# Performance work log

Measured on AMD Instinct MI355X. Metric: run time of the kernel, lower is better.

Reference implementation:

```python
import jax, jax.numpy as jnp
import numpy as np

B, D = 512, 512

def setup_inputs() -> dict:
    key = jax.random.key(0)
    k1, k2, k3, k4 = jax.random.split(key, 4)
    return {
        "img_proj": jax.random.normal(k1, (B, D), dtype=jnp.float32),
        "audio_proj": jax.random.normal(k2, (B, D), dtype=jnp.float32),
        "W": jax.random.normal(k3, (D, D), dtype=jnp.float32) * 0.02,
        "b": jax.random.normal(k4, (D,), dtype=jnp.float32) * 0.02,
    }

def reference(img_proj, audio_proj, W, b):
    # concat of raw projections (saved before img_proj is transformed)
    concat_proj = jnp.concatenate([img_proj, audio_proj], axis=-1)  # [B, 2D]
    # linear + tanh on image projection
    img_t = jnp.tanh(img_proj @ W.T + b)                            # [B, D]
    # rank-1 bilinear co-attention map: L[b,i,j] = img_t[b,i] * audio[b,j]
    L = img_t[:, :, None] * audio_proj[:, None, :]                  # [B, D, D]
    # softmax over dim=1 (rows), attend audio: C_img[b,e] = sum_d audio[b,d] * S1[b,e,d]
    S1 = jax.nn.softmax(L, axis=1)
    C_img = jnp.einsum('bd,bed->be', audio_proj, S1)                # [B, D]
    # softmax over dim=2 (cols), attend tanh-image: C_audio[b,e] = sum_d img_t[b,d] * S2[b,d,e]
    S2 = jax.nn.softmax(L, axis=2)
    C_audio = jnp.einsum('bd,bde->be', img_t, S2)                   # [B, D]
    fused = jnp.concatenate([C_img, C_audio], axis=-1)              # [B, 2D]
    return jnp.concatenate([concat_proj, fused], axis=-1)           # [B, 4D]
```

## Files before the change

### kernel.cpp

```cpp
#include <hip/hip_runtime.h>

#define K_TERMS 24

#define INVF_INIT { \
  1.0f, 1.0f, 0.5f, 1.6666666666666666e-01f, 4.1666666666666664e-02f, \
  8.3333333333333332e-03f, 1.3888888888888889e-03f, 1.9841269841269841e-04f, \
  2.4801587301587302e-05f, 2.7557319223985893e-06f, 2.7557319223985888e-07f, \
  2.5052108385441720e-08f, 2.0876756987868098e-09f, 1.6059043836821613e-10f, \
  1.1470745597729725e-11f, 7.6471637318198164e-13f, 4.7794773323873852e-14f, \
  2.8114572543455206e-15f, 1.5619206968586225e-16f, 8.2206352466243295e-18f, \
  4.1103176233121648e-19f, 1.9572941063391263e-20f, 8.8967913924505741e-22f, \
  3.8681701706306835e-23f }

__global__ __launch_bounds__(256) void transpose_w(const float* __restrict__ W,
                                                   float* __restrict__ Wt) {
  __shared__ float tile[32][33];
  const int bx = blockIdx.x, by = blockIdx.y;
  const int c = threadIdx.x & 31, r0 = threadIdx.x >> 5;
#pragma unroll
  for (int i = 0; i < 4; ++i) {
    const int r = r0 + 8 * i;
    tile[r][c] = W[(by * 32 + r) * 512 + bx * 32 + c];
  }
  __syncthreads();
#pragma unroll
  for (int i = 0; i < 4; ++i) {
    const int r = r0 + 8 * i;
    Wt[(bx * 32 + r) * 512 + by * 32 + c] = tile[c][r];
  }
}

template <bool HAS_WT>
__global__ __launch_bounds__(512) void fused_kernel(
    const float* __restrict__ img, const float* __restrict__ audio,
    const float* __restrict__ W, const float* __restrict__ bias,
    const float* __restrict__ Wt, float* __restrict__ out) {
  const int tid = threadIdx.x;
  const int b0 = blockIdx.x * 2;

  __shared__ float aL[2][512];
  __shared__ float tL[2][512];
  __shared__ float cwL[2][512];
  __shared__ float rwL[2][512];
  __shared__ float red[4][128][8];
  __shared__ float gT[2][K_TERMS], gA[2][K_TERMS];
  __shared__ float gS[2][K_TERMS], gR[2][K_TERMS];

  constexpr float INVF[K_TERMS] = INVF_INIT;

#pragma unroll
  for (int s = tid; s < 1024; s += 512) {
    const int r = s >> 9, i = s & 511;
    const float iv = img[(size_t)(b0 + r) * 512 + i];
    const float av = audio[(size_t)(b0 + r) * 512 + i];
    out[(size_t)(b0 + r) * 2048 + i] = iv;
    out[(size_t)(b0 + r) * 2048 + 512 + i] = av;
    aL[r][i] = av;
  }

  {
    const int q = tid & 127;
    const int kh = tid >> 7;
    const int kbase = __builtin_amdgcn_readfirstlane(kh) * 128;
    float4 acc0 = {0.f, 0.f, 0.f, 0.f};
    float4 acc1 = {0.f, 0.f, 0.f, 0.f};
    const float* i0p = img + (size_t)b0 * 512;
    const float* i1p = img + (size_t)(b0 + 1) * 512;
    for (int kk = 0; kk < 128; kk += 4) {
      const int k = kbase + kk;
      const float4 iv0 = *(const float4*)(i0p + k);
      const float4 iv1 = *(const float4*)(i1p + k);
      const float im0[4] = {iv0.x, iv0.y, iv0.z, iv0.w};
      const float im1[4] = {iv1.x, iv1.y, iv1.z, iv1.w};
#pragma unroll
      for (int u = 0; u < 4; ++u) {
        float4 w4;
        if (HAS_WT) {
          w4 = *(const float4*)(Wt + (size_t)(k + u) * 512 + 4 * q);
        } else {
          w4.x = W[(size_t)(4 * q + 0) * 512 + k + u];
          w4.y = W[(size_t)(4 * q + 1) * 512 + k + u];
          w4.z = W[(size_t)(4 * q + 2) * 512 + k + u];
          w4.w = W[(size_t)(4 * q + 3) * 512 + k + u];
        }
        acc0.x = fmaf(w4.x, im0[u], acc0.x);
        acc0.y = fmaf(w4.y, im0[u], acc0.y);
        acc0.z = fmaf(w4.z, im0[u], acc0.z);
        acc0.w = fmaf(w4.w, im0[u], acc0.w);
        acc1.x = fmaf(w4.x, im1[u], acc1.x);
        acc1.y = fmaf(w4.y, im1[u], acc1.y);
        acc1.z = fmaf(w4.z, im1[u], acc1.z);
        acc1.w = fmaf(w4.w, im1[u], acc1.w);
      }
    }
    *(float4*)&red[kh][q][0] = acc0;
    *(float4*)&red[kh][q][4] = acc1;
  }
  __syncthreads();
#pragma unroll
  for (int s = tid; s < 1024; s += 512) {
    const int q = s >> 3, c = s & 7;
    const int r = c >> 2, e = 4 * q + (c & 3);
    float v = red[0][q][c] + red[1][q][c] + red[2][q][c] + red[3][q][c];
    tL[r][e] = tanhf(v + bias[e]);
  }
  __syncthreads();

  const int wave = tid >> 6, lane = tid & 63;

  if (wave < 4) {
    const int r = wave >> 1, typ = wave & 1;
    const float* src = typ ? aL[r] : tL[r];
    float part[K_TERMS];
#pragma unroll
    for (int k = 0; k < K_TERMS; ++k) part[k] = 0.f;
#pragma unroll
    for (int u = 0; u < 8; ++u) {
      const float x = src[lane + 64 * u];
      float p = x;
      part[1] += p;
#pragma unroll
      for (int k = 2; k < K_TERMS; ++k) { p *= x; part[k] += p; }
    }
#pragma unroll
    for (int m = 1; m < 64; m <<= 1) {
#pragma unroll
      for (int k = 1; k < K_TERMS; ++k) part[k] += __shfl_xor(part[k], m, 64);
    }
    if (lane == 0) {
      float* g = typ ? gA[r] : gT[r];
      g[0] = 512.0f;
#pragma unroll
      for (int k = 1; k < K_TERMS; ++k) g[k] = part[k] * INVF[k];
    }
  }
  __syncthreads();

  {
    const int grp = tid >> 7, e0 = tid & 127;
    const int r = grp >> 1, kind = grp & 1;
    float g[K_TERMS];
    const float* gsrc = kind ? gA[r] : gT[r];
#pragma unroll
    for (int k = 0; k < K_TERMS; ++k) g[k] = gsrc[k];
    const float* xs = kind ? tL[r] : aL[r];
    float* dst = kind ? rwL[r] : cwL[r];
#pragma unroll
    for (int u = 0; u < 4; ++u) {
      const int e = e0 + 128 * u;
      const float x = xs[e];
      float s = g[K_TERMS - 1];
#pragma unroll
      for (int k = K_TERMS - 2; k >= 0; --k) s = fmaf(s, x, g[k]);
      dst[e] = x / s;
    }
  }
  __syncthreads();

  if (wave < 4) {
    const int r = wave >> 1, typ = wave & 1;
    const float* xs = typ ? tL[r] : aL[r];
    const float* ws = typ ? rwL[r] : cwL[r];
    float part[K_TERMS];
#pragma unroll
    for (int k = 0; k < K_TERMS; ++k) part[k] = 0.f;
#pragma unroll
    for (int u = 0; u < 8; ++u) {
      const int i = lane + 64 * u;
      const float x = xs[i];
      float p = ws[i];
      part[0] += p;
#pragma unroll
      for (int k = 1; k < K_TERMS; ++k) { p *= x; part[k] += p; }
    }
#pragma unroll
    for (int m = 1; m < 64; m <<= 1) {
#pragma unroll
      for (int k = 0; k < K_TERMS; ++k) part[k] += __shfl_xor(part[k], m, 64);
    }
    if (lane == 0) {
      float* g = typ ? gR[r] : gS[r];
#pragma unroll
      for (int k = 0; k < K_TERMS; ++k) g[k] = part[k] * INVF[k];
    }
  }
  __syncthreads();

  {
    const int grp = tid >> 7, e0 = tid & 127;
    const int r = grp >> 1, kind = grp & 1;
    float g[K_TERMS];
    const float* gsrc = kind ? gR[r] : gS[r];
#pragma unroll
    for (int k = 0; k < K_TERMS; ++k) g[k] = gsrc[k];
    const float* xs = kind ? aL[r] : tL[r];
    float* op = out + (size_t)(b0 + r) * 2048 + 1024 + kind * 512;
#pragma unroll
    for (int u = 0; u < 4; ++u) {
      const int e = e0 + 128 * u;
      const float x = xs[e];
      float s = g[K_TERMS - 1];
#pragma unroll
      for (int k = K_TERMS - 2; k >= 0; --k) s = fmaf(s, x, g[k]);
      op[e] = s;
    }
  }
}

extern "C" void kernel_launch(void* const* d_in, const int* in_sizes, int n_in,
                              void* d_out, int out_size, void* d_ws, size_t ws_size,
                              hipStream_t stream) {
  const float* img   = (const float*)d_in[0];
  const float* audio = (const float*)d_in[1];
  const float* W     = (const float*)d_in[2];
  const float* bias  = (const float*)d_in[3];
  float* out = (float*)d_out;
  float* Wt = (float*)d_ws;

  if (ws_size >= (size_t)(1 << 20)) {
    hipLaunchKernelGGL(transpose_w, dim3(16, 16), dim3(256), 0, stream, W, Wt);
    hipLaunchKernelGGL((fused_kernel<true>), dim3(256), dim3(512), 0, stream,
                       img, audio, W, bias, Wt, out);
  } else {
    hipLaunchKernelGGL((fused_kernel<false>), dim3(256), dim3(512), 0, stream,
                       img, audio, W, bias, (const float*)nullptr, out);
  }
}
```

Baseline: 79.39 us.

## Split GEMM+tanh into separate bf16 MFMA kernel feeding the moments kernel

Moves the img@W^T + bias + tanh computation out of the fused per-row kernel into a standalone tiled GEMM kernel using bf16 MFMA 16x16x32 instructions, writing tanh results to workspace (or the output buffer). The moments kernel then just loads the precomputed tanh row instead of each block re-streaming all of W. This removes the W transpose pass and the redundant per-block full-W reads, at the cost of bf16 rounding of inputs and weights, which lowers GEMM precision.

```diff
diff --git a/kernel.cpp b/kernel.cpp
--- a/kernel.cpp
+++ b/kernel.cpp
@@ -12,29 +12,65 @@
   4.1103176233121648e-19f, 1.9572941063391263e-20f, 8.8967913924505741e-22f, \
   3.8681701706306835e-23f }
 
-__global__ __launch_bounds__(256) void transpose_w(const float* __restrict__ W,
-                                                   float* __restrict__ Wt) {
-  __shared__ float tile[32][33];
-  const int bx = blockIdx.x, by = blockIdx.y;
-  const int c = threadIdx.x & 31, r0 = threadIdx.x >> 5;
+typedef __attribute__((ext_vector_type(4))) float floatx4;
+typedef __attribute__((ext_vector_type(8))) short short8;
+
+__device__ __forceinline__ unsigned short f2bf_rn(float f) {
+  union { float f; unsigned u; } v; v.f = f;
+  const unsigned r = v.u + 0x7FFFu + ((v.u >> 16) & 1u);
+  return (unsigned short)(r >> 16);
+}
+
+__global__ __launch_bounds__(256) void gemm_tanh_mfma(
+    const float* __restrict__ img, const float* __restrict__ W,
+    const float* __restrict__ bias, float* __restrict__ tdst, int tstride) {
+  __shared__ unsigned short Abf[32][40];
+  __shared__ unsigned short Wbf[32][40];
+  const int tid = threadIdx.x;
+  const int bx = blockIdx.x;
+  const int by = blockIdx.y;
+  const int r  = tid >> 3;
+  const int c4 = (tid & 7) * 4;
+  const int lane = tid & 63;
+  const int wv = tid >> 6;
+  const int bm = (wv >> 1) * 16;
+  const int en = (wv & 1) * 16;
+  const int frow = lane & 15;
+  const int kg = lane >> 4;
+
+  floatx4 acc = {0.f, 0.f, 0.f, 0.f};
+  const float* aprow = img + (size_t)(by * 32 + r) * 512;
+  const float* wprow = W   + (size_t)(bx * 32 + r) * 512;
+
+  for (int k0 = 0; k0 < 512; k0 += 32) {
+    const float4 av = *(const float4*)(aprow + k0 + c4);
+    const float4 wl = *(const float4*)(wprow + k0 + c4);
+    __syncthreads();
+    ushort4 ab, wb;
+    ab.x = f2bf_rn(av.x); ab.y = f2bf_rn(av.y);
+    ab.z = f2bf_rn(av.z); ab.w = f2bf_rn(av.w);
+    wb.x = f2bf_rn(wl.x); wb.y = f2bf_rn(wl.y);
+    wb.z = f2bf_rn(wl.z); wb.w = f2bf_rn(wl.w);
+    *(ushort4*)&Abf[r][c4] = ab;
+    *(ushort4*)&Wbf[r][c4] = wb;
+    __syncthreads();
+    const short8 afrag = *(const short8*)&Abf[bm + frow][kg * 8];
+    const short8 wfrag = *(const short8*)&Wbf[en + frow][kg * 8];
+    acc = __builtin_amdgcn_mfma_f32_16x16x32_bf16(afrag, wfrag, acc, 0, 0, 0);
+  }
+
+  const int e = bx * 32 + en + frow;
+  const float bv = bias[e];
+  const int b_base = by * 32 + bm + kg * 4;
 #pragma unroll
   for (int i = 0; i < 4; ++i) {
-    const int r = r0 + 8 * i;
-    tile[r][c] = W[(by * 32 + r) * 512 + bx * 32 + c];
-  }
-  __syncthreads();
-#pragma unroll
-  for (int i = 0; i < 4; ++i) {
-    const int r = r0 + 8 * i;
-    Wt[(bx * 32 + r) * 512 + by * 32 + c] = tile[c][r];
-  }
-}
-
-template <bool HAS_WT>
-__global__ __launch_bounds__(512) void fused_kernel(
+    tdst[(size_t)(b_base + i) * tstride + e] = tanhf(acc[i] + bv);
+  }
+}
+
+__global__ __launch_bounds__(512) void coattn_moments(
     const float* __restrict__ img, const float* __restrict__ audio,
-    const float* __restrict__ W, const float* __restrict__ bias,
-    const float* __restrict__ Wt, float* __restrict__ out) {
+    const float* __restrict__ tsrc, int tstride, float* __restrict__ out) {
   const int tid = threadIdx.x;
   const int b0 = blockIdx.x * 2;
 
@@ -42,7 +78,6 @@
   __shared__ float tL[2][512];
   __shared__ float cwL[2][512];
   __shared__ float rwL[2][512];
-  __shared__ float red[4][128][8];
   __shared__ float gT[2][K_TERMS], gA[2][K_TERMS];
   __shared__ float gS[2][K_TERMS], gR[2][K_TERMS];
 
@@ -56,53 +91,7 @@
     out[(size_t)(b0 + r) * 2048 + i] = iv;
     out[(size_t)(b0 + r) * 2048 + 512 + i] = av;
     aL[r][i] = av;
-  }
-
-  {
-    const int q = tid & 127;
-    const int kh = tid >> 7;
-    const int kbase = __builtin_amdgcn_readfirstlane(kh) * 128;
-    float4 acc0 = {0.f, 0.f, 0.f, 0.f};
-    float4 acc1 = {0.f, 0.f, 0.f, 0.f};
-    const float* i0p = img + (size_t)b0 * 512;
-    const float* i1p = img + (size_t)(b0 + 1) * 512;
-    for (int kk = 0; kk < 128; kk += 4) {
-      const int k = kbase + kk;
-      const float4 iv0 = *(const float4*)(i0p + k);
-      const float4 iv1 = *(const float4*)(i1p + k);
-      const float im0[4] = {iv0.x, iv0.y, iv0.z, iv0.w};
-      const float im1[4] = {iv1.x, iv1.y, iv1.z, iv1.w};
-#pragma unroll
-      for (int u = 0; u < 4; ++u) {
-        float4 w4;
-        if (HAS_WT) {
-          w4 = *(const float4*)(Wt + (size_t)(k + u) * 512 + 4 * q);
-        } else {
-          w4.x = W[(size_t)(4 * q + 0) * 512 + k + u];
-          w4.y = W[(size_t)(4 * q + 1) * 512 + k + u];
-          w4.z = W[(size_t)(4 * q + 2) * 512 + k + u];
-          w4.w = W[(size_t)(4 * q + 3) * 512 + k + u];
-        }
-        acc0.x = fmaf(w4.x, im0[u], acc0.x);
-        acc0.y = fmaf(w4.y, im0[u], acc0.y);
-        acc0.z = fmaf(w4.z, im0[u], acc0.z);
-        acc0.w = fmaf(w4.w, im0[u], acc0.w);
-        acc1.x = fmaf(w4.x, im1[u], acc1.x);
-        acc1.y = fmaf(w4.y, im1[u], acc1.y);
-        acc1.z = fmaf(w4.z, im1[u], acc1.z);
-        acc1.w = fmaf(w4.w, im1[u], acc1.w);
-      }
-    }
-    *(float4*)&red[kh][q][0] = acc0;
-    *(float4*)&red[kh][q][4] = acc1;
-  }
-  __syncthreads();
-#pragma unroll
-  for (int s = tid; s < 1024; s += 512) {
-    const int q = s >> 3, c = s & 7;
-    const int r = c >> 2, e = 4 * q + (c & 3);
-    float v = red[0][q][c] + red[1][q][c] + red[2][q][c] + red[3][q][c];
-    tL[r][e] = tanhf(v + bias[e]);
+    tL[r][i] = tsrc[(size_t)(b0 + r) * tstride + i];
   }
   __syncthreads();
 
@@ -215,14 +204,19 @@
   const float* W     = (const float*)d_in[2];
   const float* bias  = (const float*)d_in[3];
   float* out = (float*)d_out;
-  float* Wt = (float*)d_ws;
-
-  if (ws_size >= (size_t)(1 << 20)) {
-    hipLaunchKernelGGL(transpose_w, dim3(16, 16), dim3(256), 0, stream, W, Wt);
-    hipLaunchKernelGGL((fused_kernel<true>), dim3(256), dim3(512), 0, stream,
-                       img, audio, W, bias, Wt, out);
+
+  float* tdst;
+  int tstride;
+  if (ws_size >= (size_t)(512 * 512 * 4)) {
+    tdst = (float*)d_ws;
+    tstride = 512;
   } else {
-    hipLaunchKernelGGL((fused_kernel<false>), dim3(256), dim3(512), 0, stream,
-                       img, audio, W, bias, (const float*)nullptr, out);
-  }
-}
+    tdst = out + 1024;
+    tstride = 2048;
+  }
+
+  hipLaunchKernelGGL(gemm_tanh_mfma, dim3(16, 16), dim3(256), 0, stream,
+                     img, W, bias, tdst, tstride);
+  hipLaunchKernelGGL(coattn_moments, dim3(256), dim3(512), 0, stream,
+                     img, audio, tdst, tstride, out);
+}
```

After: 76.25 us. -3.9%, faster.
